# Kernel tuning notes

Measured on AMD Instinct MI355X. Metric: run time of the kernel, lower is better.

The kernel has to match this reference:

```python
import jax, jax.numpy as jnp
import numpy as np

VOCAB = 50000
EMB = 1024
HID = 1024
H = HID // 2            # per-direction hidden size
NTAG = 34
START = 32
STOP = 33
SEQ = 4096
NEG = -10000.0


def setup_inputs() -> dict:
    key = jax.random.key(0)
    ks = jax.random.split(key, 16)
    s = 0.05

    def rn(k, shape, scale=1.0):
        return (jax.random.normal(k, shape) * scale).astype(jnp.float32)

    logT = jax.random.normal(ks[12], (NTAG, NTAG)).astype(jnp.float32)
    logT = logT.at[START, :].set(NEG).at[:, STOP].set(NEG)
    return {
        "sentence": jax.random.randint(ks[0], (SEQ,), 0, VOCAB),
        "embed": rn(ks[1], (VOCAB, EMB), s),
        "w_ih_f": rn(ks[2], (4 * H, EMB), s), "w_hh_f": rn(ks[3], (4 * H, H), s),
        "b_ih_f": rn(ks[4], (4 * H,), s), "b_hh_f": rn(ks[5], (4 * H,), s),
        "w_ih_b": rn(ks[6], (4 * H, EMB), s), "w_hh_b": rn(ks[7], (4 * H, H), s),
        "b_ih_b": rn(ks[8], (4 * H,), s), "b_hh_b": rn(ks[9], (4 * H,), s),
        "W_out": rn(ks[10], (NTAG, HID), s), "b_out": rn(ks[11], (NTAG,), s),
        "log_transitions": logT,
        "h0": rn(ks[13], (2, H)),
        "c0": rn(ks[14], (2, H)),
    }


def _lstm(xg, w_hh, h0, c0):
    # xg: [S, 4H] precomputed input-side gate preactivations (incl. both biases)
    def step(carry, g_x):
        h, c = carry
        g = g_x + h @ w_hh.T
        i, f, gg, o = jnp.split(g, 4)          # torch gate order: i, f, g, o
        i = jax.nn.sigmoid(i)
        f = jax.nn.sigmoid(f)
        gg = jnp.tanh(gg)
        o = jax.nn.sigmoid(o)
        c = f * c + i * gg
        h = o * jnp.tanh(c)
        return (h, c), h
    _, hs = jax.lax.scan(step, (h0, c0), xg)
    return hs  # [S, H]


def reference(sentence, embed, w_ih_f, w_hh_f, b_ih_f, b_hh_f,
              w_ih_b, w_hh_b, b_ih_b, b_hh_b, W_out, b_out,
              log_transitions, h0, c0):
    x = embed[sentence]                                  # [S, EMB]
    # bidirectional LSTM, batch=1
    xg_f = x @ w_ih_f.T + (b_ih_f + b_hh_f)
    hs_f = _lstm(xg_f, w_hh_f, h0[0], c0[0])             # [S, H]
    xg_b = (x @ w_ih_b.T + (b_ih_b + b_hh_b))[::-1]
    hs_b = _lstm(xg_b, w_hh_b, h0[1], c0[1])[::-1]       # [S, H]
    feats = jnp.concatenate([hs_f, hs_b], -1) @ W_out.T + b_out  # [S, NTAG]

    # Viterbi decode (single fused scan instead of per-step host loop)
    init = jnp.full((NTAG,), NEG, jnp.float32).at[START].set(0.0)

    def vstep(fv, feat):
        scores = fv[None, :] + log_transitions           # [next, prev]
        bp = jnp.argmax(scores, axis=1)                  # backpointers
        return jnp.max(scores, axis=1) + feat, bp

    fv, bptrs = jax.lax.scan(vstep, init, feats)         # bptrs: [S, NTAG]
    terminal = fv + log_transitions[STOP]
    best = jnp.argmax(terminal)
    path_score = terminal[best]

    def btstep(tag, bp):
        return bp[tag], tag                              # emit tag at current t
    _, path_rev = jax.lax.scan(btstep, best, bptrs[::-1])
    best_path = path_rev[::-1]                           # [S] int tags
    return path_score, best_path
```

## Files before the change

kernel.cpp:

```cpp
#include <hip/hip_runtime.h>
#include <math.h>

#define SEQn 4096
#define EMBn 1024
#define Hn   512
#define G4n  2048
#define NTAGn 34
#define START_TAG 32
#define STOP_TAG 33
#define NEGV (-10000.0f)
#define CHL 128
#define WARM 48
#define NSTEPS_MAX (CHL + WARM)
#define VCH 64
#define VCL 64
#define VWARM 128
#define PADNEG (-1.0e30f)

typedef unsigned long long ull;
typedef __attribute__((ext_vector_type(8))) short bf16x8;
typedef __attribute__((ext_vector_type(4))) float f32x4;
typedef __attribute__((ext_vector_type(2))) _Float16 half2v;

__device__ __forceinline__ unsigned f2bf(float f) {
  unsigned u = __float_as_uint(f);
  return (u + 0x7FFFu + ((u >> 16) & 1u)) >> 16;
}

__device__ __forceinline__ half2v pkh(float a, float b) {
  auto r = __builtin_amdgcn_cvt_pkrtz(a, b);
  return __builtin_bit_cast(half2v, r);
}

#if defined(__has_builtin)
#if __has_builtin(__builtin_amdgcn_fdot2)
#define HAS_FDOT2 1
#endif
#endif

__device__ __forceinline__ float dot2acc(half2v w, half2v h, float acc) {
#ifdef HAS_FDOT2
  return __builtin_amdgcn_fdot2(w, h, acc, false);
#else
  return acc + (float)w.x * (float)h.x + (float)w.y * (float)h.y;
#endif
}

#define SEG_DOT(HSEG, A0, A1, A2, A3) do {                                  \
  half2v hp[16];                                                            \
  _Pragma("unroll") for (int jj = 0; jj < 8; ++jj) {                        \
    float4 hv = *(const float4*)((HSEG) + jj * 4);                          \
    hp[2*jj]   = pkh(hv.x, hv.y);                                           \
    hp[2*jj+1] = pkh(hv.z, hv.w);                                           \
  }                                                                         \
  _Pragma("unroll") for (int jj = 0; jj < 16; ++jj) {                       \
    A0 = dot2acc(wreg[0][jj], hp[jj], A0);                                  \
    A1 = dot2acc(wreg[1][jj], hp[jj], A1);                                  \
    A2 = dot2acc(wreg[2][jj], hp[jj], A2);                                  \
    A3 = dot2acc(wreg[3][jj], hp[jj], A3);                                  \
  }                                                                         \
} while (0)

__global__ __launch_bounds__(256) void xg_mfma_kernel(
    const int* __restrict__ sent, const float* __restrict__ embed,
    const float* __restrict__ w_f, const float* __restrict__ w_b,
    const float* __restrict__ bif, const float* __restrict__ bhf,
    const float* __restrict__ bib, const float* __restrict__ bhb,
    float* __restrict__ xgf, float* __restrict__ xgb)
{
  const int dz = blockIdx.z;
  const float* W   = dz ? w_b : w_f;
  const float* b1  = dz ? bib : bif;
  const float* b2  = dz ? bhb : bhf;
  float* C         = dz ? xgb : xgf;

  __shared__ unsigned short Alds[128 * 64];
  __shared__ unsigned short Blds[128 * 64];
  __shared__ int sent_s[128];

  const int tid = threadIdx.x;
  const int m0 = blockIdx.x * 128, n0 = blockIdx.y * 128;
  if (tid < 128) sent_s[tid] = sent[m0 + tid];

  const int w = tid >> 6, l = tid & 63;
  const int wm = w >> 1, wn = w & 1;

  const int srow = tid >> 4;
  const int scol = (tid & 15) * 4;

  f32x4 acc[4][4] = {};

  for (int kt = 0; kt < EMBn; kt += 64) {
    __syncthreads();
#pragma unroll
    for (int i = 0; i < 8; ++i) {
      int row = srow + i * 16;
      float4 va = *(const float4*)(embed + (size_t)sent_s[row] * EMBn + kt + scol);
      float4 vb = *(const float4*)(W + (size_t)(n0 + row) * EMBn + kt + scol);
      unsigned pa0 = f2bf(va.x) | (f2bf(va.y) << 16);
      unsigned pa1 = f2bf(va.z) | (f2bf(va.w) << 16);
      unsigned pb0 = f2bf(vb.x) | (f2bf(vb.y) << 16);
      unsigned pb1 = f2bf(vb.z) | (f2bf(vb.w) << 16);
      int idx = (row * 64 + scol) ^ ((row & 7) << 3);
      *(uint2*)&Alds[idx] = make_uint2(pa0, pa1);
      *(uint2*)&Blds[idx] = make_uint2(pb0, pb1);
    }
    __syncthreads();
#pragma unroll
    for (int kk = 0; kk < 2; ++kk) {
      bf16x8 af[4], bfr[4];
      const int kus = kk * 32 + (l >> 4) * 8;
#pragma unroll
      for (int mi = 0; mi < 4; ++mi) {
        int row = wm * 64 + mi * 16 + (l & 15);
        af[mi] = *(bf16x8*)&Alds[(row * 64 + kus) ^ ((row & 7) << 3)];
      }
#pragma unroll
      for (int ni = 0; ni < 4; ++ni) {
        int row = wn * 64 + ni * 16 + (l & 15);
        bfr[ni] = *(bf16x8*)&Blds[(row * 64 + kus) ^ ((row & 7) << 3)];
      }
#pragma unroll
      for (int mi = 0; mi < 4; ++mi)
#pragma unroll
        for (int ni = 0; ni < 4; ++ni)
          acc[mi][ni] = __builtin_amdgcn_mfma_f32_16x16x32_bf16(
              af[mi], bfr[ni], acc[mi][ni], 0, 0, 0);
    }
  }

  const int cm = m0 + wm * 64 + (l >> 4) * 4;
  const int cn = n0 + wn * 64 + (l & 15);
#pragma unroll
  for (int ni = 0; ni < 4; ++ni) {
    float bv = b1[cn + ni * 16] + b2[cn + ni * 16];
#pragma unroll
    for (int mi = 0; mi < 4; ++mi)
#pragma unroll
      for (int r = 0; r < 4; ++r)
        C[(size_t)(cm + mi * 16 + r) * G4n + cn + ni * 16] = acc[mi][ni][r] + bv;
  }
}

__global__ __launch_bounds__(1024) void lstm_kernel(
    const float* __restrict__ xg_f, const float* __restrict__ xg_b,
    const float* __restrict__ w_hh_f, const float* __restrict__ w_hh_b,
    const float* __restrict__ h0, const float* __restrict__ c0,
    float* __restrict__ hs, ull* __restrict__ hpair)
{
  const int bid = blockIdx.x;
  const int g = bid >> 3;
  const int blk = bid & 7;
  const int dir = g & 1;
  const int m = g >> 1;
  const int cA = 2 * m, cB = 2 * m + 1;
  const int warmA = cA ? WARM : 0;
  const int nstepsA = CHL + warmA;
  const int s0A = dir ? (SEQn - 1 - cA * CHL + warmA) : (cA * CHL - warmA);
  const int s0B = dir ? (SEQn - 1 - cB * CHL + WARM) : (cB * CHL - WARM);

  const int hbase = blk * 64;
  const float* W  = dir ? w_hh_b : w_hh_f;
  const float* xg = dir ? xg_b : xg_f;
  ull* pairsA = hpair + (size_t)(dir * 32 + cA) * 4 * Hn;
  ull* pairsB = hpair + (size_t)(dir * 32 + cB) * 4 * Hn;

  const int t = threadIdx.x;
  const int w = t >> 6;
  const int l = t & 63;
  const bool isTW = (w == 2 * blk);

  half2v wreg[4][16];
#pragma unroll
  for (int q = 0; q < 4; ++q) {
    const float* wrow = W + (size_t)(q * Hn + hbase + l) * Hn + w * 32;
#pragma unroll
    for (int jj = 0; jj < 8; ++jj) {
      float4 v = *(const float4*)(wrow + jj * 4);
      wreg[q][2 * jj]     = pkh(v.x, v.y);
      wreg[q][2 * jj + 1] = pkh(v.z, v.w);
    }
  }

  __shared__ __align__(16) float h_ldsA[Hn];
  __shared__ __align__(16) float h_ldsB[Hn];
  __shared__ float part[2][16 * 256];

  if (isTW) __builtin_amdgcn_s_setprio(1);

  float c_regA = 0.f, c_regB = 0.f;
  float xgcA[4] = {}, xgnA[4] = {}, xgcB[4] = {}, xgnB[4] = {};
  if (isTW) {
    if (cA == 0) c_regA = c0[dir * Hn + hbase + l];
#pragma unroll
    for (int q = 0; q < 4; ++q) {
      xgcA[q] = xg[(size_t)s0A * G4n + q * Hn + hbase + l];
      xgcB[q] = xg[(size_t)s0B * G4n + q * Hn + hbase + l];
    }
  }
  if (l < 32) {
    h_ldsA[w * 32 + l] = (cA == 0) ? h0[dir * Hn + w * 32 + l] : 0.f;
    h_ldsB[w * 32 + l] = 0.f;
  }

  for (int k = 0; k < NSTEPS_MAX; ++k) {
    const bool doA = (k < nstepsA);

    if (doA) {
      if (isTW && (k + 1 < nstepsA)) {
        const int s1 = dir ? (s0A - k - 1) : (s0A + k + 1);
#pragma unroll
        for (int q = 0; q < 4; ++q)
          xgnA[q] = xg[(size_t)s1 * G4n + q * Hn + hbase + l];
      }
      if (!isTW && k > 0 && l < 32) {
        ull* p = pairsA + (size_t)(k & 3) * Hn + w * 32 + l;
        ull v;
        do {
          v = __hip_atomic_load(p, __ATOMIC_RELAXED, __HIP_MEMORY_SCOPE_AGENT);
        } while ((unsigned)(v >> 32) != (unsigned)k);
        h_ldsA[w * 32 + l] = __uint_as_float((unsigned)v);
      }
      float a0 = 0.f, a1 = 0.f, a2 = 0.f, a3 = 0.f;
      SEG_DOT(h_ldsA + w * 32, a0, a1, a2, a3);
      part[0][w * 256 + l]       = a0;
      part[0][w * 256 + 64 + l]  = a1;
      part[0][w * 256 + 128 + l] = a2;
      part[0][w * 256 + 192 + l] = a3;
    }
    __syncthreads();

    if (doA && isTW) {
      float g0 = xgcA[0], g1 = xgcA[1], g2 = xgcA[2], g3 = xgcA[3];
#pragma unroll
      for (int ww = 0; ww < 16; ++ww) {
        g0 += part[0][ww * 256 + l];
        g1 += part[0][ww * 256 + 64 + l];
        g2 += part[0][ww * 256 + 128 + l];
        g3 += part[0][ww * 256 + 192 + l];
      }
      float iv = 1.f / (1.f + __expf(-g0));
      float fv = 1.f / (1.f + __expf(-g1));
      float gg = 2.f / (1.f + __expf(-2.f * g2)) - 1.f;
      float ov = 1.f / (1.f + __expf(-g3));
      float c = fv * c_regA + iv * gg;
      c_regA = c;
      float e2 = __expf(-2.f * c);
      float h = ov * (1.f - e2) / (1.f + e2);
      if (k + 1 < nstepsA) {
        ull pv = ((ull)(unsigned)(k + 1) << 32) | (ull)__float_as_uint(h);
        __hip_atomic_store(pairsA + (size_t)((k + 1) & 3) * Hn + hbase + l, pv,
                           __ATOMIC_RELAXED, __HIP_MEMORY_SCOPE_AGENT);
      }
      if (l < 32) h_ldsA[hbase + l] = h;
      if (k >= warmA) {
        const int s = dir ? (s0A - k) : (s0A + k);
        hs[(size_t)s * 1024 + dir * Hn + hbase + l] = h;
      }
#pragma unroll
      for (int q = 0; q < 4; ++q) xgcA[q] = xgnA[q];
    }

    {
      if (isTW && (k + 1 < NSTEPS_MAX)) {
        const int s1 = dir ? (s0B - k - 1) : (s0B + k + 1);
#pragma unroll
        for (int q = 0; q < 4; ++q)
          xgnB[q] = xg[(size_t)s1 * G4n + q * Hn + hbase + l];
      }
      if (!isTW && k > 0 && l < 32) {
        ull* p = pairsB + (size_t)(k & 3) * Hn + w * 32 + l;
        ull v;
        do {
          v = __hip_atomic_load(p, __ATOMIC_RELAXED, __HIP_MEMORY_SCOPE_AGENT);
        } while ((unsigned)(v >> 32) != (unsigned)k);
        h_ldsB[w * 32 + l] = __uint_as_float((unsigned)v);
      }
      float a0 = 0.f, a1 = 0.f, a2 = 0.f, a3 = 0.f;
      SEG_DOT(h_ldsB + w * 32, a0, a1, a2, a3);
      part[1][w * 256 + l]       = a0;
      part[1][w * 256 + 64 + l]  = a1;
      part[1][w * 256 + 128 + l] = a2;
      part[1][w * 256 + 192 + l] = a3;
    }
    __syncthreads();

    if (isTW) {
      float g0 = xgcB[0], g1 = xgcB[1], g2 = xgcB[2], g3 = xgcB[3];
#pragma unroll
      for (int ww = 0; ww < 16; ++ww) {
        g0 += part[1][ww * 256 + l];
        g1 += part[1][ww * 256 + 64 + l];
        g2 += part[1][ww * 256 + 128 + l];
        g3 += part[1][ww * 256 + 192 + l];
      }
      float iv = 1.f / (1.f + __expf(-g0));
      float fv = 1.f / (1.f + __expf(-g1));
      float gg = 2.f / (1.f + __expf(-2.f * g2)) - 1.f;
      float ov = 1.f / (1.f + __expf(-g3));
      float c = fv * c_regB + iv * gg;
      c_regB = c;
      float e2 = __expf(-2.f * c);
      float h = ov * (1.f - e2) / (1.f + e2);
      if (k + 1 < NSTEPS_MAX) {
        ull pv = ((ull)(unsigned)(k + 1) << 32) | (ull)__float_as_uint(h);
        __hip_atomic_store(pairsB + (size_t)((k + 1) & 3) * Hn + hbase + l, pv,
                           __ATOMIC_RELAXED, __HIP_MEMORY_SCOPE_AGENT);
      }
      if (l < 32) h_ldsB[hbase + l] = h;
      if (k >= WARM) {
        const int s = dir ? (s0B - k) : (s0B + k);
        hs[(size_t)s * 1024 + dir * Hn + hbase + l] = h;
      }
#pragma unroll
      for (int q = 0; q < 4; ++q) xgcB[q] = xgnB[q];
    }
  }
}

__global__ __launch_bounds__(256) void feats_mfma_kernel(
    const float* __restrict__ hs, const float* __restrict__ W_out,
    const float* __restrict__ b_out, float* __restrict__ feats)
{
  __shared__ unsigned short Alds[128 * 64];
  __shared__ unsigned short Blds[48 * 64];

  const int tid = threadIdx.x;
  const int m0 = blockIdx.x * 128;
  const int w = tid >> 6, l = tid & 63;

  const int srow = tid >> 4;
  const int scol = (tid & 15) * 4;

  f32x4 acc[2][3] = {};

  for (int kt = 0; kt < 1024; kt += 64) {
    __syncthreads();
#pragma unroll
    for (int i = 0; i < 8; ++i) {
      int row = srow + i * 16;
      float4 va = *(const float4*)(hs + (size_t)(m0 + row) * 1024 + kt + scol);
      unsigned pa0 = f2bf(va.x) | (f2bf(va.y) << 16);
      unsigned pa1 = f2bf(va.z) | (f2bf(va.w) << 16);
      int idx = (row * 64 + scol) ^ ((row & 7) << 3);
      *(uint2*)&Alds[idx] = make_uint2(pa0, pa1);
    }
#pragma unroll
    for (int i = 0; i < 3; ++i) {
      int row = srow + i * 16;
      uint2 pb = make_uint2(0u, 0u);
      if (row < NTAGn) {
        float4 vb = *(const float4*)(W_out + (size_t)row * 1024 + kt + scol);
        pb.x = f2bf(vb.x) | (f2bf(vb.y) << 16);
        pb.y = f2bf(vb.z) | (f2bf(vb.w) << 16);
      }
      int idx = (row * 64 + scol) ^ ((row & 7) << 3);
      *(uint2*)&Blds[idx] = pb;
    }
    __syncthreads();
#pragma unroll
    for (int kk = 0; kk < 2; ++kk) {
      const int kus = kk * 32 + (l >> 4) * 8;
      bf16x8 af[2], bfr[3];
#pragma unroll
      for (int mi = 0; mi < 2; ++mi) {
        int row = w * 32 + mi * 16 + (l & 15);
        af[mi] = *(bf16x8*)&Alds[(row * 64 + kus) ^ ((row & 7) << 3)];
      }
#pragma unroll
      for (int ni = 0; ni < 3; ++ni) {
        int row = ni * 16 + (l & 15);
        bfr[ni] = *(bf16x8*)&Blds[(row * 64 + kus) ^ ((row & 7) << 3)];
      }
#pragma unroll
      for (int mi = 0; mi < 2; ++mi)
#pragma unroll
        for (int ni = 0; ni < 3; ++ni)
          acc[mi][ni] = __builtin_amdgcn_mfma_f32_16x16x32_bf16(
              af[mi], bfr[ni], acc[mi][ni], 0, 0, 0);
    }
  }

  const int cm = m0 + w * 32 + (l >> 4) * 4;
  const int cn = l & 15;
#pragma unroll
  for (int ni = 0; ni < 3; ++ni) {
    int col = cn + ni * 16;
    if (col < NTAGn) {
      float bv = b_out[col];
#pragma unroll
      for (int mi = 0; mi < 2; ++mi)
#pragma unroll
        for (int r = 0; r < 4; ++r)
          feats[(size_t)(cm + mi * 16 + r) * NTAGn + col] = acc[mi][ni][r] + bv;
    }
  }
}

__global__ __launch_bounds__(64) void vit_chunk(
    const float* __restrict__ feats, const float* __restrict__ logT,
    unsigned char* __restrict__ pstore, int* __restrict__ Eg,
    float* __restrict__ fvfin)
{
  const int c = blockIdx.x;
  const int lane = threadIdx.x;
  const int start = c * VCL;
  const int wstart = (start - VWARM > 0) ? (start - VWARM) : 0;
  const int warm = start - wstart;
  const bool exact = (wstart == 0);
  const int nsteps = warm + VCL;

  __shared__ __align__(16) float fv_s[36];
  __shared__ unsigned char bpl[VCL][36];
  __shared__ __align__(16) float fl[VWARM + VCL][36];
  const bool active = lane < NTAGn;

  float Trow[36];
  if (active) {
#pragma unroll
    for (int j = 0; j < NTAGn; ++j) Trow[j] = logT[lane * NTAGn + j];
    Trow[34] = PADNEG; Trow[35] = PADNEG;
  }
  for (int x = lane; x < nsteps * NTAGn; x += 64) {
    int s = x / NTAGn, j = x - s * NTAGn;
    fl[s][j] = feats[(size_t)wstart * NTAGn + x];
  }
  if (lane < 36) {
    float init;
    if (exact) init = (lane == START_TAG) ? 0.f : ((lane < NTAGn) ? NEGV : PADNEG);
    else       init = (lane < NTAGn) ? 0.f : PADNEG;
    fv_s[lane] = init;
  }
  __syncthreads();

  for (int s = 0; s < nsteps; ++s) {
    float best = -3.4e38f; int bj = 0;
    if (active) {
      float sc[36];
#pragma unroll
      for (int q = 0; q < 9; ++q) {
        float4 f4 = *(const float4*)&fv_s[q * 4];
        sc[q*4+0] = f4.x + Trow[q*4+0];
        sc[q*4+1] = f4.y + Trow[q*4+1];
        sc[q*4+2] = f4.z + Trow[q*4+2];
        sc[q*4+3] = f4.w + Trow[q*4+3];
      }
      best = sc[0];
#pragma unroll
      for (int j = 1; j < 36; ++j) { if (sc[j] > best) { best = sc[j]; bj = j; } }
    }
    if (active) {
      fv_s[lane] = best + fl[s][lane];
      if (s >= warm) bpl[s - warm][lane] = (unsigned char)bj;
    }
    __threadfence_block();
  }
  __syncthreads();

  if (c == VCH - 1 && lane < 36) fvfin[lane] = fv_s[lane];

  if (active) {
    int p = lane;
    unsigned char* ps = pstore + ((size_t)c * NTAGn + lane) * VCL;
    for (int s = VCL - 1; s >= 1; --s) {
      ps[s] = (unsigned char)p;
      p = bpl[s][p];
    }
    ps[0] = (unsigned char)p;
    Eg[c * NTAGn + lane] = bpl[0][p];
  }
}

__global__ __launch_bounds__(64) void vit_final(
    const float* __restrict__ feats, const float* __restrict__ logT,
    const float* __restrict__ fvfin, const unsigned char* __restrict__ pstore,
    const int* __restrict__ Eg, float* __restrict__ out)
{
  const int lane = threadIdx.x;
  __shared__ float term[64];
  __shared__ int ec[VCH];
  __shared__ unsigned char path_lds[SEQn];

  term[lane] = (lane < NTAGn)
             ? (fvfin[lane] + logT[STOP_TAG * NTAGn + lane]) : -3.4e38f;
  __syncthreads();
  if (lane == 0) {
    float bv = -3.4e38f; int bi = 0;
#pragma unroll
    for (int i = 0; i < NTAGn; ++i) { if (term[i] > bv) { bv = term[i]; bi = i; } }
    int e = bi;
    for (int c = VCH - 1; c >= 1; --c) { ec[c] = e; e = Eg[c * NTAGn + e]; }
    ec[0] = e;
  }
  __syncthreads();
  for (int t = lane; t < SEQn; t += 64) {
    int c = t >> 6;
    unsigned char p = pstore[((size_t)c * NTAGn + ec[c]) * VCL + (t & 63)];
    path_lds[t] = p;
    out[1 + t] = (float)p;
  }
  __syncthreads();

  float s = 0.f;
  for (int t = lane; t < SEQn; t += 64) {
    int p = path_lds[t];
    int pp = (t == 0) ? START_TAG : (int)path_lds[t - 1];
    s += feats[(size_t)t * NTAGn + p] + logT[p * NTAGn + pp];
  }
#pragma unroll
  for (int off = 32; off; off >>= 1) s += __shfl_xor(s, off);
  if (lane == 0)
    out[0] = s + logT[STOP_TAG * NTAGn + (int)path_lds[SEQn - 1]];
}

extern "C" void kernel_launch(void* const* d_in, const int* in_sizes, int n_in,
                              void* d_out, int out_size, void* d_ws, size_t ws_size,
                              hipStream_t stream) {
  const int*   sent   = (const int*)d_in[0];
  const float* embed  = (const float*)d_in[1];
  const float* w_ih_f = (const float*)d_in[2];
  const float* w_hh_f = (const float*)d_in[3];
  const float* b_ih_f = (const float*)d_in[4];
  const float* b_hh_f = (const float*)d_in[5];
  const float* w_ih_b = (const float*)d_in[6];
  const float* w_hh_b = (const float*)d_in[7];
  const float* b_ih_b = (const float*)d_in[8];
  const float* b_hh_b = (const float*)d_in[9];
  const float* W_out  = (const float*)d_in[10];
  const float* b_out  = (const float*)d_in[11];
  const float* logT   = (const float*)d_in[12];
  const float* h0     = (const float*)d_in[13];
  const float* c0     = (const float*)d_in[14];
  float* out = (float*)d_out;

  char* ws = (char*)d_ws;
  size_t off = 0;
  float* xg_f  = (float*)(ws + off); off += (size_t)SEQn * G4n * 4;
  float* xg_b  = (float*)(ws + off); off += (size_t)SEQn * G4n * 4;
  float* hs    = (float*)(ws + off); off += (size_t)SEQn * 1024 * 4;
  float* feats = (float*)(ws + off); off += (size_t)SEQn * NTAGn * 4;
  ull*   hpair = (ull*)(ws + off);   off += (size_t)64 * 4 * Hn * 8;
  unsigned char* pstore = (unsigned char*)(ws + off); off += (size_t)VCH * NTAGn * VCL;
  int*   Eg    = (int*)(ws + off);   off += (size_t)VCH * NTAGn * 4;
  float* fvfin = (float*)(ws + off); off += 64 * 4;

  (void)hipMemsetAsync(hpair, 0, (size_t)64 * 4 * Hn * 8, stream);

  dim3 gg(SEQn / 128, G4n / 128, 2);
  xg_mfma_kernel<<<gg, 256, 0, stream>>>(sent, embed, w_ih_f, w_ih_b,
                                         b_ih_f, b_hh_f, b_ih_b, b_hh_b,
                                         xg_f, xg_b);

  lstm_kernel<<<256, 1024, 0, stream>>>(xg_f, xg_b, w_hh_f, w_hh_b, h0, c0,
                                        hs, hpair);

  feats_mfma_kernel<<<SEQn / 128, 256, 0, stream>>>(hs, W_out, b_out, feats);

  vit_chunk<<<VCH, 64, 0, stream>>>(feats, logT, pstore, Eg, fvfin);
  vit_final<<<1, 64, 0, stream>>>(feats, logT, fvfin, pstore, Eg, out);
}
```

Measured before the change: 751.7 us.

## Interleave four shorter LSTM chunks per block group instead of two

Halves the LSTM chunk length and has each 8-block group advance four independent chunk recurrences in round-robin phases, doubling the number of chunks and the handoff buffer. The intent is to hide cross-block h exchange latency behind more independent work and shorten the sequential step count. It increases redundant warmup work, total phases, and LDS usage for partial sums.

```diff
diff --git a/kernel.cpp b/kernel.cpp
--- a/kernel.cpp
+++ b/kernel.cpp
@@ -9,7 +9,7 @@
 #define START_TAG 32
 #define STOP_TAG 33
 #define NEGV (-10000.0f)
-#define CHL 128
+#define CHL 64
 #define WARM 48
 #define NSTEPS_MAX (CHL + WARM)
 #define VCH 64
@@ -61,6 +61,61 @@
   }                                                                         \
 } while (0)
 
+#define LSTM_PHASE(X, IDX)                                                  \
+  {                                                                         \
+    const bool doX = (k < nsteps##X);                                       \
+    if (doX) {                                                              \
+      if (isTW && (k + 1 < nsteps##X)) {                                    \
+        const int s1 = dir ? (s0##X - k - 1) : (s0##X + k + 1);             \
+        _Pragma("unroll") for (int q = 0; q < 4; ++q)                       \
+          xgn##X[q] = xg[(size_t)s1 * G4n + q * Hn + hbase + l];            \
+      }                                                                     \
+      if (!isTW && k > 0 && l < 32) {                                       \
+        ull* p = pairs##X + (size_t)(k & 3) * Hn + w * 32 + l;              \
+        ull v;                                                              \
+        do {                                                                \
+          v = __hip_atomic_load(p, __ATOMIC_RELAXED, __HIP_MEMORY_SCOPE_AGENT); \
+        } while ((unsigned)(v >> 32) != (unsigned)k);                       \
+        h_lds##X[w * 32 + l] = __uint_as_float((unsigned)v);                \
+      }                                                                     \
+      float a0 = 0.f, a1 = 0.f, a2 = 0.f, a3 = 0.f;                         \
+      SEG_DOT(h_lds##X + w * 32, a0, a1, a2, a3);                           \
+      part[IDX][w * 256 + l]       = a0;                                    \
+      part[IDX][w * 256 + 64 + l]  = a1;                                    \
+      part[IDX][w * 256 + 128 + l] = a2;                                    \
+      part[IDX][w * 256 + 192 + l] = a3;                                    \
+    }                                                                       \
+    __syncthreads();                                                        \
+    if (doX && isTW) {                                                      \
+      float g0 = xgc##X[0], g1 = xgc##X[1], g2 = xgc##X[2], g3 = xgc##X[3]; \
+      _Pragma("unroll") for (int ww = 0; ww < 16; ++ww) {                   \
+        g0 += part[IDX][ww * 256 + l];                                      \
+        g1 += part[IDX][ww * 256 + 64 + l];                                 \
+        g2 += part[IDX][ww * 256 + 128 + l];                                \
+        g3 += part[IDX][ww * 256 + 192 + l];                                \
+      }                                                                     \
+      float iv = 1.f / (1.f + __expf(-g0));                                 \
+      float fv = 1.f / (1.f + __expf(-g1));                                 \
+      float gg = 2.f / (1.f + __expf(-2.f * g2)) - 1.f;                     \
+      float ov = 1.f / (1.f + __expf(-g3));                                 \
+      float c = fv * c_reg##X + iv * gg;                                    \
+      c_reg##X = c;                                                         \
+      float e2 = __expf(-2.f * c);                                          \
+      float h = ov * (1.f - e2) / (1.f + e2);                               \
+      if (k + 1 < nsteps##X) {                                              \
+        ull pv = ((ull)(unsigned)(k + 1) << 32) | (ull)__float_as_uint(h);  \
+        __hip_atomic_store(pairs##X + (size_t)((k + 1) & 3) * Hn + hbase + l, \
+                           pv, __ATOMIC_RELAXED, __HIP_MEMORY_SCOPE_AGENT); \
+      }                                                                     \
+      if (l < 32) h_lds##X[hbase + l] = h;                                  \
+      if (k >= warm##X) {                                                   \
+        const int s = dir ? (s0##X - k) : (s0##X + k);                      \
+        hs[(size_t)s * 1024 + dir * Hn + hbase + l] = h;                    \
+      }                                                                     \
+      _Pragma("unroll") for (int q = 0; q < 4; ++q) xgc##X[q] = xgn##X[q];  \
+    }                                                                       \
+  }
+
 __global__ __launch_bounds__(256) void xg_mfma_kernel(
     const int* __restrict__ sent, const float* __restrict__ embed,
     const float* __restrict__ w_f, const float* __restrict__ w_b,
@@ -153,17 +208,23 @@
   const int blk = bid & 7;
   const int dir = g & 1;
   const int m = g >> 1;
-  const int cA = 2 * m, cB = 2 * m + 1;
+  const int cA = 4 * m, cB = 4 * m + 1, cC = 4 * m + 2, cD = 4 * m + 3;
   const int warmA = cA ? WARM : 0;
+  const int warmB = WARM, warmC = WARM, warmD = WARM;
   const int nstepsA = CHL + warmA;
+  const int nstepsB = NSTEPS_MAX, nstepsC = NSTEPS_MAX, nstepsD = NSTEPS_MAX;
   const int s0A = dir ? (SEQn - 1 - cA * CHL + warmA) : (cA * CHL - warmA);
   const int s0B = dir ? (SEQn - 1 - cB * CHL + WARM) : (cB * CHL - WARM);
+  const int s0C = dir ? (SEQn - 1 - cC * CHL + WARM) : (cC * CHL - WARM);
+  const int s0D = dir ? (SEQn - 1 - cD * CHL + WARM) : (cD * CHL - WARM);
 
   const int hbase = blk * 64;
   const float* W  = dir ? w_hh_b : w_hh_f;
   const float* xg = dir ? xg_b : xg_f;
-  ull* pairsA = hpair + (size_t)(dir * 32 + cA) * 4 * Hn;
-  ull* pairsB = hpair + (size_t)(dir * 32 + cB) * 4 * Hn;
+  ull* pairsA = hpair + (size_t)(dir * 64 + cA) * 4 * Hn;
+  ull* pairsB = hpair + (size_t)(dir * 64 + cB) * 4 * Hn;
+  ull* pairsC = hpair + (size_t)(dir * 64 + cC) * 4 * Hn;
+  ull* pairsD = hpair + (size_t)(dir * 64 + cD) * 4 * Hn;
 
   const int t = threadIdx.x;
   const int w = t >> 6;
@@ -184,137 +245,37 @@
 
   __shared__ __align__(16) float h_ldsA[Hn];
   __shared__ __align__(16) float h_ldsB[Hn];
-  __shared__ float part[2][16 * 256];
+  __shared__ __align__(16) float h_ldsC[Hn];
+  __shared__ __align__(16) float h_ldsD[Hn];
+  __shared__ float part[4][16 * 256];
 
   if (isTW) __builtin_amdgcn_s_setprio(1);
 
-  float c_regA = 0.f, c_regB = 0.f;
+  float c_regA = 0.f, c_regB = 0.f, c_regC = 0.f, c_regD = 0.f;
   float xgcA[4] = {}, xgnA[4] = {}, xgcB[4] = {}, xgnB[4] = {};
+  float xgcC[4] = {}, xgnC[4] = {}, xgcD[4] = {}, xgnD[4] = {};
   if (isTW) {
     if (cA == 0) c_regA = c0[dir * Hn + hbase + l];
 #pragma unroll
     for (int q = 0; q < 4; ++q) {
       xgcA[q] = xg[(size_t)s0A * G4n + q * Hn + hbase + l];
       xgcB[q] = xg[(size_t)s0B * G4n + q * Hn + hbase + l];
+      xgcC[q] = xg[(size_t)s0C * G4n + q * Hn + hbase + l];
+      xgcD[q] = xg[(size_t)s0D * G4n + q * Hn + hbase + l];
     }
   }
   if (l < 32) {
     h_ldsA[w * 32 + l] = (cA == 0) ? h0[dir * Hn + w * 32 + l] : 0.f;
     h_ldsB[w * 32 + l] = 0.f;
+    h_ldsC[w * 32 + l] = 0.f;
+    h_ldsD[w * 32 + l] = 0.f;
   }
 
   for (int k = 0; k < NSTEPS_MAX; ++k) {
-    const bool doA = (k < nstepsA);
-
-    if (doA) {
-      if (isTW && (k + 1 < nstepsA)) {
-        const int s1 = dir ? (s0A - k - 1) : (s0A + k + 1);
-#pragma unroll
-        for (int q = 0; q < 4; ++q)
-          xgnA[q] = xg[(size_t)s1 * G4n + q * Hn + hbase + l];
-      }
-      if (!isTW && k > 0 && l < 32) {
-        ull* p = pairsA + (size_t)(k & 3) * Hn + w * 32 + l;
-        ull v;
-        do {
-          v = __hip_atomic_load(p, __ATOMIC_RELAXED, __HIP_MEMORY_SCOPE_AGENT);
-        } while ((unsigned)(v >> 32) != (unsigned)k);
-        h_ldsA[w * 32 + l] = __uint_as_float((unsigned)v);
-      }
-      float a0 = 0.f, a1 = 0.f, a2 = 0.f, a3 = 0.f;
-      SEG_DOT(h_ldsA + w * 32, a0, a1, a2, a3);
-      part[0][w * 256 + l]       = a0;
-      part[0][w * 256 + 64 + l]  = a1;
-      part[0][w * 256 + 128 + l] = a2;
-      part[0][w * 256 + 192 + l] = a3;
-    }
-    __syncthreads();
-
-    if (doA && isTW) {
-      float g0 = xgcA[0], g1 = xgcA[1], g2 = xgcA[2], g3 = xgcA[3];
-#pragma unroll
-      for (int ww = 0; ww < 16; ++ww) {
-        g0 += part[0][ww * 256 + l];
-        g1 += part[0][ww * 256 + 64 + l];
-        g2 += part[0][ww * 256 + 128 + l];
-        g3 += part[0][ww * 256 + 192 + l];
-      }
-      float iv = 1.f / (1.f + __expf(-g0));
-      float fv = 1.f / (1.f + __expf(-g1));
-      float gg = 2.f / (1.f + __expf(-2.f * g2)) - 1.f;
-      float ov = 1.f / (1.f + __expf(-g3));
-      float c = fv * c_regA + iv * gg;
-      c_regA = c;
-      float e2 = __expf(-2.f * c);
-      float h = ov * (1.f - e2) / (1.f + e2);
-      if (k + 1 < nstepsA) {
-        ull pv = ((ull)(unsigned)(k + 1) << 32) | (ull)__float_as_uint(h);
-        __hip_atomic_store(pairsA + (size_t)((k + 1) & 3) * Hn + hbase + l, pv,
-                           __ATOMIC_RELAXED, __HIP_MEMORY_SCOPE_AGENT);
-      }
-      if (l < 32) h_ldsA[hbase + l] = h;
-      if (k >= warmA) {
-        const int s = dir ? (s0A - k) : (s0A + k);
-        hs[(size_t)s * 1024 + dir * Hn + hbase + l] = h;
-      }
-#pragma unroll
-      for (int q = 0; q < 4; ++q) xgcA[q] = xgnA[q];
-    }
-
-    {
-      if (isTW && (k + 1 < NSTEPS_MAX)) {
-        const int s1 = dir ? (s0B - k - 1) : (s0B + k + 1);
-#pragma unroll
-        for (int q = 0; q < 4; ++q)
-          xgnB[q] = xg[(size_t)s1 * G4n + q * Hn + hbase + l];
-      }
-      if (!isTW && k > 0 && l < 32) {
-        ull* p = pairsB + (size_t)(k & 3) * Hn + w * 32 + l;
-        ull v;
-        do {
-          v = __hip_atomic_load(p, __ATOMIC_RELAXED, __HIP_MEMORY_SCOPE_AGENT);
-        } while ((unsigned)(v >> 32) != (unsigned)k);
-        h_ldsB[w * 32 + l] = __uint_as_float((unsigned)v);
-      }
-      float a0 = 0.f, a1 = 0.f, a2 = 0.f, a3 = 0.f;
-      SEG_DOT(h_ldsB + w * 32, a0, a1, a2, a3);
-      part[1][w * 256 + l]       = a0;
-      part[1][w * 256 + 64 + l]  = a1;
-      part[1][w * 256 + 128 + l] = a2;
-      part[1][w * 256 + 192 + l] = a3;
-    }
-    __syncthreads();
-
-    if (isTW) {
-      float g0 = xgcB[0], g1 = xgcB[1], g2 = xgcB[2], g3 = xgcB[3];
-#pragma unroll
-      for (int ww = 0; ww < 16; ++ww) {
-        g0 += part[1][ww * 256 + l];
-        g1 += part[1][ww * 256 + 64 + l];
-        g2 += part[1][ww * 256 + 128 + l];
-        g3 += part[1][ww * 256 + 192 + l];
-      }
-      float iv = 1.f / (1.f + __expf(-g0));
-      float fv = 1.f / (1.f + __expf(-g1));
-      float gg = 2.f / (1.f + __expf(-2.f * g2)) - 1.f;
-      float ov = 1.f / (1.f + __expf(-g3));
-      float c = fv * c_regB + iv * gg;
-      c_regB = c;
-      float e2 = __expf(-2.f * c);
-      float h = ov * (1.f - e2) / (1.f + e2);
-      if (k + 1 < NSTEPS_MAX) {
-        ull pv = ((ull)(unsigned)(k + 1) << 32) | (ull)__float_as_uint(h);
-        __hip_atomic_store(pairsB + (size_t)((k + 1) & 3) * Hn + hbase + l, pv,
-                           __ATOMIC_RELAXED, __HIP_MEMORY_SCOPE_AGENT);
-      }
-      if (l < 32) h_ldsB[hbase + l] = h;
-      if (k >= WARM) {
-        const int s = dir ? (s0B - k) : (s0B + k);
-        hs[(size_t)s * 1024 + dir * Hn + hbase + l] = h;
-      }
-#pragma unroll
-      for (int q = 0; q < 4; ++q) xgcB[q] = xgnB[q];
-    }
+    LSTM_PHASE(A, 0)
+    LSTM_PHASE(B, 1)
+    LSTM_PHASE(C, 2)
+    LSTM_PHASE(D, 3)
   }
 }
 
@@ -539,12 +500,12 @@
   float* xg_b  = (float*)(ws + off); off += (size_t)SEQn * G4n * 4;
   float* hs    = (float*)(ws + off); off += (size_t)SEQn * 1024 * 4;
   float* feats = (float*)(ws + off); off += (size_t)SEQn * NTAGn * 4;
-  ull*   hpair = (ull*)(ws + off);   off += (size_t)64 * 4 * Hn * 8;
+  ull*   hpair = (ull*)(ws + off);   off += (size_t)128 * 4 * Hn * 8;
   unsigned char* pstore = (unsigned char*)(ws + off); off += (size_t)VCH * NTAGn * VCL;
   int*   Eg    = (int*)(ws + off);   off += (size_t)VCH * NTAGn * 4;
   float* fvfin = (float*)(ws + off); off += 64 * 4;
 
-  (void)hipMemsetAsync(hpair, 0, (size_t)64 * 4 * Hn * 8, stream);
+  (void)hipMemsetAsync(hpair, 0, (size_t)128 * 4 * Hn * 8, stream);
 
   dim3 gg(SEQn / 128, G4n / 128, 2);
   xg_mfma_kernel<<<gg, 256, 0, stream>>>(sent, embed, w_ih_f, w_ih_b,
```

Result: slower. 1.270 ms (+69.0%).
